# Kernel tuning notes

Hardware: AMD Instinct MI355X
Metric: run time of the kernel (lower is better)

The kernel has to match this reference:

```python
import jax, jax.numpy as jnp
import numpy as np

NUM_HEADS = 8
EPS = 1e-9


def setup_inputs() -> dict:
    key = jax.random.key(0)
    ks = jax.random.split(key, 8)
    B, N, D = 2, 2048, 512
    s = 1.0 / np.sqrt(D)
    x = jax.random.normal(ks[0], (B, N, D), dtype=jnp.float32)
    adjacency = jax.random.uniform(ks[1], (B, N, N), dtype=jnp.float32)
    # Linear weights stored as (in, out) so application is x @ W + b
    W_q = jax.random.normal(ks[2], (D, D), dtype=jnp.float32) * s
    W_k = jax.random.normal(ks[3], (D, D), dtype=jnp.float32) * s
    W_v = jax.random.normal(ks[4], (D, D), dtype=jnp.float32) * s
    b_q = jnp.zeros((D,), jnp.float32)
    b_k = jnp.zeros((D,), jnp.float32)
    b_v = jnp.zeros((D,), jnp.float32)
    # soul_gate: Linear(2D -> 1); weight stored as flat (2D,), bias scalar
    w_g = jax.random.normal(ks[5], (2 * D,), dtype=jnp.float32) * (1.0 / np.sqrt(2 * D))
    b_g = jnp.zeros((), jnp.float32)
    return {"x": x, "adjacency": adjacency, "W_q": W_q, "b_q": b_q,
            "W_k": W_k, "b_k": b_k, "W_v": W_v, "b_v": b_v,
            "w_g": w_g, "b_g": b_g}


def reference(x, adjacency, W_q, b_q, W_k, b_k, W_v, b_v, w_g, b_g):
    B, N, D = x.shape
    H = NUM_HEADS
    hd = D // H
    Q = (x @ W_q + b_q).reshape(B, N, H, hd)
    K = (x @ W_k + b_k).reshape(B, N, H, hd)
    V = (x @ W_v + b_v).reshape(B, N, H, hd)
    scores = jnp.einsum('bihd,bjhd->bhij', Q, K) / jnp.sqrt(jnp.float32(hd))
    # soul_gate(cat[x_i, x_j]) is linear, so it decomposes exactly:
    # bias[b,i,j] = x[b,i]@w_g[:D] + x[b,j]@w_g[D:] + b_g  (same math, no (B,N,N,2D) tensor)
    a = x @ w_g[:D]          # (B, N) contribution of x_i
    c = x @ w_g[D:]          # (B, N) contribution of x_j
    soul_bias = a[:, :, None] + c[:, None, :] + b_g   # (B, N, N)
    scores = scores + (soul_bias + jnp.log(adjacency + EPS))[:, None, :, :]
    attn = jax.nn.softmax(scores, axis=-1)            # (B, H, N, N)
    out = jnp.einsum('bhij,bjhd->bihd', attn, V).reshape(B, N, D)
    return out + x
```

## Files before the change

kernel.cpp:

```cpp
#include <hip/hip_runtime.h>
#include <hip/hip_bf16.h>

typedef __bf16 bf16x8 __attribute__((ext_vector_type(8)));
typedef float f32x4 __attribute__((ext_vector_type(4)));
typedef unsigned short u16x8 __attribute__((ext_vector_type(8)));

#define LOG2E 1.44269504f

__device__ __forceinline__ unsigned short f2bu(float f) {
    __hip_bfloat16 h = __float2bfloat16(f);
    unsigned short u;
    __builtin_memcpy(&u, &h, 2);
    return u;
}

__device__ __forceinline__ float fexp2(float x) {
#if __has_builtin(__builtin_amdgcn_exp2f)
    return __builtin_amdgcn_exp2f(x);
#else
    return __expf(x * 0.69314718f);
#endif
}

__device__ __forceinline__ float bu2f(unsigned short u) {
    unsigned int v = ((unsigned int)u) << 16;
    float f;
    __builtin_memcpy(&f, &v, 4);
    return f;
}

#define GLDS16(gp, lp) __builtin_amdgcn_global_load_lds( \
    (const __attribute__((address_space(1))) unsigned int*)(gp), \
    (__attribute__((address_space(3))) unsigned int*)(lp), 16, 0, 0)

#define OFF_QS  0u
#define OFF_KB  4194304u
#define OFF_VT  8388608u
#define OFF_CV  12582912u
#define OFF_XB  12599296u
#define OFF_WT  16793600u
#define OFF_MQ  18366464u

__global__ void k_prepwt(const float* __restrict__ x, const float* __restrict__ wg,
                         const float* __restrict__ w0, const float* __restrict__ w1,
                         const float* __restrict__ w2,
                         unsigned short* __restrict__ xb, float* __restrict__ cv2,
                         unsigned short* __restrict__ wt) {
    if (blockIdx.x < 1024) {
        int row = blockIdx.x * 4 + (threadIdx.x >> 6);
        int l = threadIdx.x & 63;
        const float4* xr = reinterpret_cast<const float4*>(x + (size_t)row * 512);
        float4 a = xr[l * 2], b2 = xr[l * 2 + 1];
        ushort4 o0, o1;
        o0.x = f2bu(a.x);  o0.y = f2bu(a.y);  o0.z = f2bu(a.z);  o0.w = f2bu(a.w);
        o1.x = f2bu(b2.x); o1.y = f2bu(b2.y); o1.z = f2bu(b2.z); o1.w = f2bu(b2.w);
        ushort4* dst = reinterpret_cast<ushort4*>(xb + (size_t)row * 512);
        dst[l * 2] = o0; dst[l * 2 + 1] = o1;
        const float4* wr = reinterpret_cast<const float4*>(wg + 512);
        float4 g0 = wr[l * 2], g1 = wr[l * 2 + 1];
        float s = a.x * g0.x + a.y * g0.y + a.z * g0.z + a.w * g0.w
                + b2.x * g1.x + b2.y * g1.y + b2.z * g1.z + b2.w * g1.w;
#pragma unroll
        for (int off = 32; off >= 1; off >>= 1) s += __shfl_xor(s, off, 64);
        if (l == 0) cv2[row] = fexp2((s - 8.0f) * LOG2E);
    } else {
        int bid2 = blockIdx.x - 1024;
        int z = bid2 >> 6, yy = bid2 & 63;
        int k0 = (yy >> 3) * 64, n0 = (yy & 7) * 64;
        const float* W = (z == 0) ? w0 : ((z == 1) ? w1 : w2);
        __shared__ float T[64][65];
        int c = threadIdx.x & 63, r0 = threadIdx.x >> 6;
#pragma unroll
        for (int i = 0; i < 16; i++) { int r = r0 + i * 4; T[r][c] = W[(k0 + r) * 512 + n0 + c]; }
        __syncthreads();
        unsigned short* Wt = wt + z * (512 * 512);
#pragma unroll
        for (int i = 0; i < 16; i++) { int a = r0 + i * 4; Wt[(n0 + a) * 512 + k0 + c] = f2bu(T[c][a]); }
    }
}

__global__ __launch_bounds__(256) void k_mid(
    const float* __restrict__ adj, const float* __restrict__ cv2,
    unsigned short* __restrict__ mq,
    const unsigned short* __restrict__ xb, const unsigned short* __restrict__ wt,
    const float* __restrict__ bq, const float* __restrict__ bk, const float* __restrict__ bv,
    unsigned short* __restrict__ Qs, unsigned short* __restrict__ Kb,
    unsigned short* __restrict__ Vt) {
    if (blockIdx.x < 8192) {
        int blk = blockIdx.x;
        int bic = blk >> 5, jt = blk & 31;
        int b = bic >> 7, ic = bic & 127;
        int t = threadIdx.x;
        int l = t >> 2, mt = t & 3, q = l >> 4, cl = l & 15;
        int j0 = jt * 64 + 16 * mt + q * 4;
        const float4 av = *reinterpret_cast<const float4*>(
            adj + ((size_t)(b * 2048 + ic * 16 + cl)) * 2048 + j0);
        const float4 cv = *reinterpret_cast<const float4*>(cv2 + b * 2048 + j0);
        ushort4 o;
        o.x = f2bu((av.x + 1e-9f) * cv.x);
        o.y = f2bu((av.y + 1e-9f) * cv.y);
        o.z = f2bu((av.z + 1e-9f) * cv.z);
        o.w = f2bu((av.w + 1e-9f) * cv.w);
        *reinterpret_cast<ushort4*>(mq + (size_t)bic * 32768 + jt * 1024 + l * 16 + mt * 4) = o;
        return;
    }
    int gid = blockIdx.x - 8192;
    int bx = gid & 63, by = (gid >> 6) & 3, z = gid >> 8;
    __shared__ __align__(16) unsigned short As[64 * 32];
    __shared__ __align__(16) unsigned short Bs[128 * 32];
    const unsigned short* Wt = wt + z * (512 * 512);
    const float* bias = (z == 0) ? bq : ((z == 1) ? bk : bv);
    float scale = (z == 0) ? (0.125f * LOG2E) : 1.0f;
    int m0 = bx * 64, n0 = by * 128;
    int tid = threadIdx.x, w = tid >> 6, l = tid & 63;
    int q = l >> 4, cl = l & 15;
    f32x4 acc[8];
#pragma unroll
    for (int nt = 0; nt < 8; nt++)
#pragma unroll
        for (int r = 0; r < 4; r++) acc[nt][r] = 0.f;
    int arow = l >> 2, ach = (l & 3) * 8;
    for (int k0 = 0; k0 < 512; k0 += 32) {
        GLDS16(xb + (size_t)(m0 + w * 16 + arow) * 512 + k0 + ach, As + w * 512);
#pragma unroll
        for (int e = 0; e < 2; e++)
            GLDS16(Wt + (size_t)(n0 + w * 32 + e * 16 + arow) * 512 + k0 + ach, Bs + w * 1024 + e * 512);
        __syncthreads();
        bf16x8 af = *reinterpret_cast<const bf16x8*>(As + (w * 16 + cl) * 32 + q * 8);
#pragma unroll
        for (int nt = 0; nt < 8; nt++) {
            bf16x8 bf = *reinterpret_cast<const bf16x8*>(Bs + (nt * 16 + cl) * 32 + q * 8);
            acc[nt] = __builtin_amdgcn_mfma_f32_16x16x32_bf16(af, bf, acc[nt], 0, 0, 0);
        }
        __syncthreads();
    }
    if (z == 2) {
        int n_ = (m0 + w * 16 + q * 4) & 2047;
        int b_ = (m0 + w * 16) >> 11;
#pragma unroll
        for (int nt = 0; nt < 8; nt++) {
            int col = n0 + nt * 16 + cl;
            int h_ = col >> 6, d_ = col & 63;
            float bv_ = bias[col];
            ushort4 o;
            o.x = f2bu(acc[nt][0] + bv_); o.y = f2bu(acc[nt][1] + bv_);
            o.z = f2bu(acc[nt][2] + bv_); o.w = f2bu(acc[nt][3] + bv_);
            *reinterpret_cast<ushort4*>(Vt + ((size_t)((b_ * 8 + h_) * 64 + d_)) * 2048 + n_) = o;
        }
    } else {
        unsigned short* Cout = (z == 0) ? Qs : Kb;
#pragma unroll
        for (int nt = 0; nt < 8; nt++) {
            int col = n0 + nt * 16 + cl;
            float bv_ = bias[col];
#pragma unroll
            for (int r = 0; r < 4; r++) {
                int row = m0 + w * 16 + q * 4 + r;
                Cout[(size_t)row * 512 + col] = f2bu((acc[nt][r] + bv_) * scale);
            }
        }
    }
}

__global__ __launch_bounds__(256, 2) void k_attn(
    const unsigned short* __restrict__ Qs, const unsigned short* __restrict__ Kb,
    const unsigned short* __restrict__ Vt, const unsigned short* __restrict__ mq,
    const float* __restrict__ x, float* __restrict__ out) {
    __shared__ __align__(16) unsigned short Ks[4096];
    __shared__ __align__(16) unsigned short Vs[4096];
    __shared__ __align__(16) unsigned short PA[4][16 * 72];
    int bid = blockIdx.x;
    int ig = bid >> 4, h = (bid >> 1) & 7, b = bid & 1;
    int tid = threadIdx.x, w = tid >> 6, l = tid & 63, q = l >> 4, cl = l & 15;
    int i0w = ig * 64 + w * 16;
    int ic = ig * 4 + w;

    bf16x8 qf0, qf1;
    {
        const unsigned short* qp = Qs + (size_t)(b * 2048 + i0w + cl) * 512 + h * 64 + q * 8;
        qf0 = *reinterpret_cast<const bf16x8*>(qp);
        qf1 = *reinterpret_cast<const bf16x8*>(qp + 32);
    }
    bf16x8 ones;
#pragma unroll
    for (int i = 0; i < 8; i++) { unsigned short o1 = 0x3F80; __builtin_memcpy(((unsigned short*)&ones) + i, &o1, 2); }

    f32x4 O[4];
    f32x4 Osum;
#pragma unroll
    for (int nt = 0; nt < 4; nt++)
#pragma unroll
        for (int r = 0; r < 4; r++) O[nt][r] = 0.f;
#pragma unroll
    for (int r = 0; r < 4; r++) Osum[r] = 0.f;

    const unsigned short* Kh = Kb + (size_t)b * 2048 * 512 + h * 64;
    const unsigned short* Vh = Vt + ((size_t)(b * 8 + h) * 64) * 2048;
    const unsigned short* mb = mq + (size_t)(b * 128 + ic) * 32768 + l * 16;
    unsigned short* pw = &PA[w][0];
    int lrow = l >> 2, lch = (l & 3) * 8;

    for (int t = 0; t < 32; t++) {
        int jb = t * 64;
#pragma unroll
        for (int e = 0; e < 2; e++) {
            int c = w * 2 + e, kk = c >> 2, r16 = (c & 3) * 16;
            GLDS16(Kh + (size_t)(jb + r16 + lrow) * 512 + kk * 32 + lch, Ks + kk * 2048 + r16 * 32);
            GLDS16(Vh + (size_t)(r16 + lrow) * 2048 + jb + kk * 32 + lch, Vs + kk * 2048 + r16 * 32);
        }
        u16x8 mh0 = *reinterpret_cast<const u16x8*>(mb + (size_t)t * 1024);
        u16x8 mh1 = *reinterpret_cast<const u16x8*>(mb + (size_t)t * 1024 + 8);
        __syncthreads();
        f32x4 S[4];
#pragma unroll
        for (int mt = 0; mt < 4; mt++) {
#pragma unroll
            for (int r = 0; r < 4; r++) S[mt][r] = 0.f;
            bf16x8 kf0 = *reinterpret_cast<const bf16x8*>(Ks + (16 * mt + cl) * 32 + q * 8);
            bf16x8 kf1 = *reinterpret_cast<const bf16x8*>(Ks + 2048 + (16 * mt + cl) * 32 + q * 8);
            S[mt] = __builtin_amdgcn_mfma_f32_16x16x32_bf16(kf0, qf0, S[mt], 0, 0, 0);
            S[mt] = __builtin_amdgcn_mfma_f32_16x16x32_bf16(kf1, qf1, S[mt], 0, 0, 0);
        }
#pragma unroll
        for (int mt = 0; mt < 4; mt++) {
            float p0 = fexp2(S[mt][0]) * bu2f((mt < 2) ? mh0[mt * 4 + 0] : mh1[(mt - 2) * 4 + 0]);
            float p1 = fexp2(S[mt][1]) * bu2f((mt < 2) ? mh0[mt * 4 + 1] : mh1[(mt - 2) * 4 + 1]);
            float p2 = fexp2(S[mt][2]) * bu2f((mt < 2) ? mh0[mt * 4 + 2] : mh1[(mt - 2) * 4 + 2]);
            float p3 = fexp2(S[mt][3]) * bu2f((mt < 2) ? mh0[mt * 4 + 3] : mh1[(mt - 2) * 4 + 3]);
            ushort4 o;
            o.x = f2bu(p0); o.y = f2bu(p1); o.z = f2bu(p2); o.w = f2bu(p3);
            *reinterpret_cast<ushort4*>(pw + cl * 72 + 16 * mt + q * 4) = o;
        }
#pragma unroll
        for (int jc = 0; jc < 2; jc++) {
            bf16x8 pf = *reinterpret_cast<const bf16x8*>(pw + cl * 72 + jc * 32 + q * 8);
#pragma unroll
            for (int nt = 0; nt < 4; nt++) {
                bf16x8 vf = *reinterpret_cast<const bf16x8*>(Vs + jc * 2048 + (16 * nt + cl) * 32 + q * 8);
                O[nt] = __builtin_amdgcn_mfma_f32_16x16x32_bf16(pf, vf, O[nt], 0, 0, 0);
            }
            Osum = __builtin_amdgcn_mfma_f32_16x16x32_bf16(pf, ones, Osum, 0, 0, 0);
        }
        __syncthreads();
    }

#pragma unroll
    for (int r = 0; r < 4; r++) {
        float inv = 1.0f / Osum[r];
        size_t base = (size_t)(b * 2048 + i0w + q * 4 + r) * 512 + h * 64;
#pragma unroll
        for (int nt = 0; nt < 4; nt++) {
            size_t idx = base + 16 * nt + cl;
            out[idx] = O[nt][r] * inv + x[idx];
        }
    }
}

extern "C" void kernel_launch(void* const* d_in, const int* in_sizes, int n_in,
                              void* d_out, int out_size, void* d_ws, size_t ws_size,
                              hipStream_t stream) {
    const float* x   = (const float*)d_in[0];
    const float* adj = (const float*)d_in[1];
    const float* Wq  = (const float*)d_in[2];
    const float* bq  = (const float*)d_in[3];
    const float* Wk  = (const float*)d_in[4];
    const float* bk  = (const float*)d_in[5];
    const float* Wv  = (const float*)d_in[6];
    const float* bv  = (const float*)d_in[7];
    const float* wg  = (const float*)d_in[8];
    float* out = (float*)d_out;
    char* ws = (char*)d_ws;
    unsigned short* Qs = (unsigned short*)(ws + OFF_QS);
    unsigned short* Kb = (unsigned short*)(ws + OFF_KB);
    unsigned short* Vt = (unsigned short*)(ws + OFF_VT);
    float* cv2 = (float*)(ws + OFF_CV);
    unsigned short* xb = (unsigned short*)(ws + OFF_XB);
    unsigned short* wt = (unsigned short*)(ws + OFF_WT);
    unsigned short* mqp = (unsigned short*)(ws + OFF_MQ);

    k_prepwt<<<1216, 256, 0, stream>>>(x, wg, Wq, Wk, Wv, xb, cv2, wt);
    k_mid<<<8960, 256, 0, stream>>>(adj, cv2, mqp, xb, wt, bq, bk, bv, Qs, Kb, Vt);
    k_attn<<<512, 256, 0, stream>>>(Qs, Kb, Vt, mqp, x, out);
}
```

Measured before the change: 159.7 us.

## Split attention over key halves, double-buffer K/V, and add combine kernel

The attention kernel now handles 128 query rows per block (two 16-row chunks per wave), which reuses each K/V tile loaded into LDS across twice as many rows. It also splits the key dimension in two so the grid stays at 512 blocks. K/V tiles and mask values are double-buffered so the next tile is prefetched while the current one is computed. Unnormalized partial outputs are written in bf16 along with row sums, and a new combine kernel adds them, normalizes, and applies the residual. This costs an extra launch, extra global traffic, bf16 rounding of the partials, and more register pressure.

```diff
diff --git a/kernel.cpp b/kernel.cpp
--- a/kernel.cpp
+++ b/kernel.cpp
@@ -40,6 +40,8 @@
 #define OFF_XB  12599296u
 #define OFF_WT  16793600u
 #define OFF_MQ  18366464u
+#define OFF_PO  35143680u
+#define OFF_PL  43532288u
 
 __global__ void k_prepwt(const float* __restrict__ x, const float* __restrict__ wg,
                          const float* __restrict__ w0, const float* __restrict__ w1,
@@ -165,94 +167,167 @@
 __global__ __launch_bounds__(256, 2) void k_attn(
     const unsigned short* __restrict__ Qs, const unsigned short* __restrict__ Kb,
     const unsigned short* __restrict__ Vt, const unsigned short* __restrict__ mq,
-    const float* __restrict__ x, float* __restrict__ out) {
-    __shared__ __align__(16) unsigned short Ks[4096];
-    __shared__ __align__(16) unsigned short Vs[4096];
+    unsigned short* __restrict__ PO, float* __restrict__ PL) {
+    __shared__ __align__(16) unsigned short Ks[2][4096];
+    __shared__ __align__(16) unsigned short Vs[2][4096];
     __shared__ __align__(16) unsigned short PA[4][16 * 72];
     int bid = blockIdx.x;
-    int ig = bid >> 4, h = (bid >> 1) & 7, b = bid & 1;
+    int h = bid >> 6, s = bid & 63, b = s >> 5, ig = (s >> 1) & 15, js = s & 1;
     int tid = threadIdx.x, w = tid >> 6, l = tid & 63, q = l >> 4, cl = l & 15;
-    int i0w = ig * 64 + w * 16;
-    int ic = ig * 4 + w;
-
-    bf16x8 qf0, qf1;
-    {
-        const unsigned short* qp = Qs + (size_t)(b * 2048 + i0w + cl) * 512 + h * 64 + q * 8;
-        qf0 = *reinterpret_cast<const bf16x8*>(qp);
-        qf1 = *reinterpret_cast<const bf16x8*>(qp + 32);
+    int bh = b * 8 + h;
+    int ic0 = ig * 8 + w * 2;
+
+    bf16x8 qf[2][2];
+#pragma unroll
+    for (int rc = 0; rc < 2; rc++) {
+        const unsigned short* qp = Qs + (size_t)(b * 2048 + ig * 128 + w * 32 + rc * 16 + cl) * 512 + h * 64 + q * 8;
+        qf[rc][0] = *reinterpret_cast<const bf16x8*>(qp);
+        qf[rc][1] = *reinterpret_cast<const bf16x8*>(qp + 32);
     }
     bf16x8 ones;
 #pragma unroll
     for (int i = 0; i < 8; i++) { unsigned short o1 = 0x3F80; __builtin_memcpy(((unsigned short*)&ones) + i, &o1, 2); }
 
-    f32x4 O[4];
-    f32x4 Osum;
-#pragma unroll
-    for (int nt = 0; nt < 4; nt++)
-#pragma unroll
-        for (int r = 0; r < 4; r++) O[nt][r] = 0.f;
-#pragma unroll
-    for (int r = 0; r < 4; r++) Osum[r] = 0.f;
+    f32x4 O[2][4];
+    f32x4 Osum[2];
+#pragma unroll
+    for (int rc = 0; rc < 2; rc++) {
+#pragma unroll
+        for (int nt = 0; nt < 4; nt++)
+#pragma unroll
+            for (int r = 0; r < 4; r++) O[rc][nt][r] = 0.f;
+#pragma unroll
+        for (int r = 0; r < 4; r++) Osum[rc][r] = 0.f;
+    }
 
     const unsigned short* Kh = Kb + (size_t)b * 2048 * 512 + h * 64;
-    const unsigned short* Vh = Vt + ((size_t)(b * 8 + h) * 64) * 2048;
-    const unsigned short* mb = mq + (size_t)(b * 128 + ic) * 32768 + l * 16;
+    const unsigned short* Vh = Vt + ((size_t)bh * 64) * 2048;
+    const unsigned short* mb0 = mq + (size_t)(b * 128 + ic0) * 32768 + l * 16 + (size_t)(js * 16) * 1024;
+    const unsigned short* mb1 = mb0 + 32768;
     unsigned short* pw = &PA[w][0];
     int lrow = l >> 2, lch = (l & 3) * 8;
-
-    for (int t = 0; t < 32; t++) {
-        int jb = t * 64;
+    int jb0 = js * 1024;
+
+    {
+        int jb = jb0;
 #pragma unroll
         for (int e = 0; e < 2; e++) {
             int c = w * 2 + e, kk = c >> 2, r16 = (c & 3) * 16;
-            GLDS16(Kh + (size_t)(jb + r16 + lrow) * 512 + kk * 32 + lch, Ks + kk * 2048 + r16 * 32);
-            GLDS16(Vh + (size_t)(r16 + lrow) * 2048 + jb + kk * 32 + lch, Vs + kk * 2048 + r16 * 32);
-        }
-        u16x8 mh0 = *reinterpret_cast<const u16x8*>(mb + (size_t)t * 1024);
-        u16x8 mh1 = *reinterpret_cast<const u16x8*>(mb + (size_t)t * 1024 + 8);
+            GLDS16(Kh + (size_t)(jb + r16 + lrow) * 512 + kk * 32 + lch, &Ks[0][kk * 2048 + r16 * 32]);
+            GLDS16(Vh + (size_t)(r16 + lrow) * 2048 + jb + kk * 32 + lch, &Vs[0][kk * 2048 + r16 * 32]);
+        }
+    }
+    u16x8 mn[2][2];
+    mn[0][0] = *reinterpret_cast<const u16x8*>(mb0);
+    mn[0][1] = *reinterpret_cast<const u16x8*>(mb0 + 8);
+    mn[1][0] = *reinterpret_cast<const u16x8*>(mb1);
+    mn[1][1] = *reinterpret_cast<const u16x8*>(mb1 + 8);
+
+    for (int t = 0; t < 16; t++) {
+        int bufi = t & 1;
         __syncthreads();
-        f32x4 S[4];
+        if (t < 15) {
+            int jb = jb0 + (t + 1) * 64;
+#pragma unroll
+            for (int e = 0; e < 2; e++) {
+                int c = w * 2 + e, kk = c >> 2, r16 = (c & 3) * 16;
+                GLDS16(Kh + (size_t)(jb + r16 + lrow) * 512 + kk * 32 + lch, &Ks[bufi ^ 1][kk * 2048 + r16 * 32]);
+                GLDS16(Vh + (size_t)(r16 + lrow) * 2048 + jb + kk * 32 + lch, &Vs[bufi ^ 1][kk * 2048 + r16 * 32]);
+            }
+        }
+        u16x8 mc[2][2];
+        mc[0][0] = mn[0][0]; mc[0][1] = mn[0][1]; mc[1][0] = mn[1][0]; mc[1][1] = mn[1][1];
+        if (t < 15) {
+            size_t off = (size_t)(t + 1) * 1024;
+            mn[0][0] = *reinterpret_cast<const u16x8*>(mb0 + off);
+            mn[0][1] = *reinterpret_cast<const u16x8*>(mb0 + off + 8);
+            mn[1][0] = *reinterpret_cast<const u16x8*>(mb1 + off);
+            mn[1][1] = *reinterpret_cast<const u16x8*>(mb1 + off + 8);
+        }
+        bf16x8 vf[2][4];
+#pragma unroll
+        for (int jc = 0; jc < 2; jc++)
+#pragma unroll
+            for (int nt = 0; nt < 4; nt++)
+                vf[jc][nt] = *reinterpret_cast<const bf16x8*>(&Vs[bufi][jc * 2048 + (16 * nt + cl) * 32 + q * 8]);
+        f32x4 S[2][4];
+#pragma unroll
+        for (int rc = 0; rc < 2; rc++)
+#pragma unroll
+            for (int mt = 0; mt < 4; mt++)
+#pragma unroll
+                for (int r = 0; r < 4; r++) S[rc][mt][r] = 0.f;
 #pragma unroll
         for (int mt = 0; mt < 4; mt++) {
-#pragma unroll
-            for (int r = 0; r < 4; r++) S[mt][r] = 0.f;
-            bf16x8 kf0 = *reinterpret_cast<const bf16x8*>(Ks + (16 * mt + cl) * 32 + q * 8);
-            bf16x8 kf1 = *reinterpret_cast<const bf16x8*>(Ks + 2048 + (16 * mt + cl) * 32 + q * 8);
-            S[mt] = __builtin_amdgcn_mfma_f32_16x16x32_bf16(kf0, qf0, S[mt], 0, 0, 0);
-            S[mt] = __builtin_amdgcn_mfma_f32_16x16x32_bf16(kf1, qf1, S[mt], 0, 0, 0);
-        }
-#pragma unroll
-        for (int mt = 0; mt < 4; mt++) {
-            float p0 = fexp2(S[mt][0]) * bu2f((mt < 2) ? mh0[mt * 4 + 0] : mh1[(mt - 2) * 4 + 0]);
-            float p1 = fexp2(S[mt][1]) * bu2f((mt < 2) ? mh0[mt * 4 + 1] : mh1[(mt - 2) * 4 + 1]);
-            float p2 = fexp2(S[mt][2]) * bu2f((mt < 2) ? mh0[mt * 4 + 2] : mh1[(mt - 2) * 4 + 2]);
-            float p3 = fexp2(S[mt][3]) * bu2f((mt < 2) ? mh0[mt * 4 + 3] : mh1[(mt - 2) * 4 + 3]);
+            bf16x8 kf0 = *reinterpret_cast<const bf16x8*>(&Ks[bufi][(16 * mt + cl) * 32 + q * 8]);
+            bf16x8 kf1 = *reinterpret_cast<const bf16x8*>(&Ks[bufi][2048 + (16 * mt + cl) * 32 + q * 8]);
+#pragma unroll
+            for (int rc = 0; rc < 2; rc++) {
+                S[rc][mt] = __builtin_amdgcn_mfma_f32_16x16x32_bf16(kf0, qf[rc][0], S[rc][mt], 0, 0, 0);
+                S[rc][mt] = __builtin_amdgcn_mfma_f32_16x16x32_bf16(kf1, qf[rc][1], S[rc][mt], 0, 0, 0);
+            }
+        }
+#pragma unroll
+        for (int rc = 0; rc < 2; rc++) {
+#pragma unroll
+            for (int mt = 0; mt < 4; mt++) {
+                float p0 = fexp2(S[rc][mt][0]) * bu2f((mt < 2) ? mc[rc][0][mt * 4 + 0] : mc[rc][1][(mt - 2) * 4 + 0]);
+                float p1 = fexp2(S[rc][mt][1]) * bu2f((mt < 2) ? mc[rc][0][mt * 4 + 1] : mc[rc][1][(mt - 2) * 4 + 1]);
+                float p2 = fexp2(S[rc][mt][2]) * bu2f((mt < 2) ? mc[rc][0][mt * 4 + 2] : mc[rc][1][(mt - 2) * 4 + 2]);
+                float p3 = fexp2(S[rc][mt][3]) * bu2f((mt < 2) ? mc[rc][0][mt * 4 + 3] : mc[rc][1][(mt - 2) * 4 + 3]);
+                ushort4 o;
+                o.x = f2bu(p0); o.y = f2bu(p1); o.z = f2bu(p2); o.w = f2bu(p3);
+                *reinterpret_cast<ushort4*>(pw + cl * 72 + 16 * mt + q * 4) = o;
+            }
+#pragma unroll
+            for (int jc = 0; jc < 2; jc++) {
+                bf16x8 pf = *reinterpret_cast<const bf16x8*>(pw + cl * 72 + jc * 32 + q * 8);
+#pragma unroll
+                for (int nt = 0; nt < 4; nt++)
+                    O[rc][nt] = __builtin_amdgcn_mfma_f32_16x16x32_bf16(pf, vf[jc][nt], O[rc][nt], 0, 0, 0);
+                Osum[rc] = __builtin_amdgcn_mfma_f32_16x16x32_bf16(pf, ones, Osum[rc], 0, 0, 0);
+            }
+        }
+    }
+
+#pragma unroll
+    for (int rc = 0; rc < 2; rc++) {
+        size_t chunk = ((size_t)(bh * 128 + ic0 + rc)) * 2 + js;
+        unsigned short* po = PO + chunk * 1024 + l * 16;
+#pragma unroll
+        for (int r = 0; r < 4; r++) {
             ushort4 o;
-            o.x = f2bu(p0); o.y = f2bu(p1); o.z = f2bu(p2); o.w = f2bu(p3);
-            *reinterpret_cast<ushort4*>(pw + cl * 72 + 16 * mt + q * 4) = o;
-        }
-#pragma unroll
-        for (int jc = 0; jc < 2; jc++) {
-            bf16x8 pf = *reinterpret_cast<const bf16x8*>(pw + cl * 72 + jc * 32 + q * 8);
-#pragma unroll
-            for (int nt = 0; nt < 4; nt++) {
-                bf16x8 vf = *reinterpret_cast<const bf16x8*>(Vs + jc * 2048 + (16 * nt + cl) * 32 + q * 8);
-                O[nt] = __builtin_amdgcn_mfma_f32_16x16x32_bf16(pf, vf, O[nt], 0, 0, 0);
-            }
-            Osum = __builtin_amdgcn_mfma_f32_16x16x32_bf16(pf, ones, Osum, 0, 0, 0);
-        }
-        __syncthreads();
-    }
-
-#pragma unroll
-    for (int r = 0; r < 4; r++) {
-        float inv = 1.0f / Osum[r];
-        size_t base = (size_t)(b * 2048 + i0w + q * 4 + r) * 512 + h * 64;
-#pragma unroll
-        for (int nt = 0; nt < 4; nt++) {
-            size_t idx = base + 16 * nt + cl;
-            out[idx] = O[nt][r] * inv + x[idx];
-        }
+            o.x = f2bu(O[rc][0][r]); o.y = f2bu(O[rc][1][r]);
+            o.z = f2bu(O[rc][2][r]); o.w = f2bu(O[rc][3][r]);
+            *reinterpret_cast<ushort4*>(po + r * 4) = o;
+        }
+        if (cl == 0) {
+#pragma unroll
+            for (int r = 0; r < 4; r++)
+                PL[chunk * 16 + q * 4 + r] = Osum[rc][r];
+        }
+    }
+}
+
+__global__ void k_comb(const unsigned short* __restrict__ PO, const float* __restrict__ PL,
+                       const float* __restrict__ x, float* __restrict__ out) {
+    int blk = blockIdx.x;
+    int t64 = blk & 31, bh = blk >> 5;
+    int b = bh >> 3, h = bh & 7;
+    int t = threadIdx.x;
+    int l = t >> 2, r = t & 3, q = l >> 4, cl = l & 15;
+#pragma unroll
+    for (int w = 0; w < 4; w++) {
+        int ic = t64 * 4 + w;
+        size_t c0 = ((size_t)(bh * 128 + ic)) * 2;
+        ushort4 a = *reinterpret_cast<const ushort4*>(PO + c0 * 1024 + t * 4);
+        ushort4 c = *reinterpret_cast<const ushort4*>(PO + (c0 + 1) * 1024 + t * 4);
+        float inv = 1.0f / (PL[c0 * 16 + q * 4 + r] + PL[c0 * 16 + 16 + q * 4 + r]);
+        size_t gro = (size_t)(b * 2048 + ic * 16 + q * 4 + r) * 512 + h * 64;
+        out[gro + 0 * 16 + cl] = (bu2f(a.x) + bu2f(c.x)) * inv + x[gro + 0 * 16 + cl];
+        out[gro + 1 * 16 + cl] = (bu2f(a.y) + bu2f(c.y)) * inv + x[gro + 1 * 16 + cl];
+        out[gro + 2 * 16 + cl] = (bu2f(a.z) + bu2f(c.z)) * inv + x[gro + 2 * 16 + cl];
+        out[gro + 3 * 16 + cl] = (bu2f(a.w) + bu2f(c.w)) * inv + x[gro + 3 * 16 + cl];
     }
 }
 
@@ -277,8 +352,11 @@
     unsigned short* xb = (unsigned short*)(ws + OFF_XB);
     unsigned short* wt = (unsigned short*)(ws + OFF_WT);
     unsigned short* mqp = (unsigned short*)(ws + OFF_MQ);
+    unsigned short* PO = (unsigned short*)(ws + OFF_PO);
+    float* PL = (float*)(ws + OFF_PL);
 
     k_prepwt<<<1216, 256, 0, stream>>>(x, wg, Wq, Wk, Wv, xb, cv2, wt);
     k_mid<<<8960, 256, 0, stream>>>(adj, cv2, mqp, xb, wt, bq, bk, bv, Qs, Kb, Vt);
-    k_attn<<<512, 256, 0, stream>>>(Qs, Kb, Vt, mqp, x, out);
-}
+    k_attn<<<512, 256, 0, stream>>>(Qs, Kb, Vt, mqp, PO, PL);
+    k_comb<<<512, 256, 0, stream>>>(PO, PL, x, out);
+}
```

Result: no change. 159.1 us (-0.4%).
